# Kernel optimization log

Hardware: AMD Instinct MI355X
Metric: run time of the kernel (lower is better)

## Reference

```python
import jax, jax.numpy as jnp
import numpy as np

B, N, K = 4, 4096, 16
D_IN, D_T = 64, 128


def _linear_params(key, d_in, d_out, scale=0.02):
    kw, kb = jax.random.split(key)
    w = jax.random.normal(kw, (d_in, d_out), dtype=jnp.float32) * scale
    b = jax.random.normal(kb, (d_out,), dtype=jnp.float32) * scale
    return w, b


def setup_inputs() -> dict:
    key = jax.random.key(0)
    ks = jax.random.split(key, 12)
    x = jax.random.normal(ks[0], (B, N, D_IN), dtype=jnp.float32)
    pos = jax.random.normal(ks[1], (B, N, 3), dtype=jnp.float32)
    fc1_w, fc1_b = _linear_params(ks[2], D_IN, D_T)
    fc2_w, fc2_b = _linear_params(ks[3], D_T, D_IN)
    d1_w, d1_b = _linear_params(ks[4], 3, D_T)
    d2_w, d2_b = _linear_params(ks[5], D_T, D_T)
    g1_w, g1_b = _linear_params(ks[6], D_T, D_T)
    g2_w, g2_b = _linear_params(ks[7], D_T, D_T)
    wq = jax.random.normal(ks[8], (D_T, D_T), dtype=jnp.float32) * 0.02
    wk = jax.random.normal(ks[9], (D_T, D_T), dtype=jnp.float32) * 0.02
    wv = jax.random.normal(ks[10], (D_T, D_T), dtype=jnp.float32) * 0.02
    return dict(x=x, pos=pos, fc1_w=fc1_w, fc1_b=fc1_b, fc2_w=fc2_w, fc2_b=fc2_b,
                d1_w=d1_w, d1_b=d1_b, d2_w=d2_w, d2_b=d2_b,
                g1_w=g1_w, g1_b=g1_b, g2_w=g2_w, g2_b=g2_b,
                wq=wq, wk=wk, wv=wv)


def reference(x, pos, fc1_w, fc1_b, fc2_w, fc2_b, d1_w, d1_b, d2_w, d2_b,
              g1_w, g1_b, g2_w, g2_b, wq, wk, wv):
    # square_distance(pos, pos): [B, N, N]
    sq = jnp.sum(pos * pos, axis=-1)
    dists = sq[:, :, None] + sq[:, None, :] - 2.0 * jnp.einsum('bnc,bmc->bnm', pos, pos)
    knn_idx = jnp.argsort(dists, axis=-1)[:, :, :K]  # [B, N, K] int
    bidx = jnp.arange(B)[:, None, None]

    knn_pos = pos[bidx, knn_idx]                     # [B, N, K, 3]
    h = x @ fc1_w + fc1_b                            # [B, N, D_T]
    q = h @ wq                                       # [B, N, D_T]
    k = (h @ wk)[bidx, knn_idx]                      # [B, N, K, D_T]
    v = (h @ wv)[bidx, knn_idx]                      # [B, N, K, D_T]

    rel = pos[:, :, None, :] - knn_pos               # [B, N, K, 3]
    pos_enc = jax.nn.relu(rel @ d1_w + d1_b) @ d2_w + d2_b  # fc_delta

    a_in = q[:, :, None, :] - k + pos_enc
    attn = jax.nn.relu(a_in @ g1_w + g1_b) @ g2_w + g2_b    # fc_gamma
    attn = jax.nn.softmax(attn / np.sqrt(D_T).astype(np.float32), axis=-2)

    res = jnp.einsum('bmnf,bmnf->bmf', attn, v + pos_enc)   # [B, N, D_T]
    out = res @ fc2_w + fc2_b + x                           # [B, N, D_IN]
    return out, attn
```

## Files before the change

### kernel.cpp

```cpp
#include <hip/hip_runtime.h>
#include <float.h>

#define NPTS 4096
#define BN   16384
#define DT   128
#define DIN  64

typedef short v8s __attribute__((ext_vector_type(8)));
typedef float v4f __attribute__((ext_vector_type(4)));

__device__ __forceinline__ unsigned short f2bf(float f) {
    union { float f; unsigned u; } v; v.f = f;
    unsigned r = v.u + 0x7fff + ((v.u >> 16) & 1);
    return (unsigned short)(r >> 16);
}
__device__ __forceinline__ float bf2f(unsigned short s) {
    union { unsigned u; float f; } v; v.u = ((unsigned)s) << 16;
    return v.f;
}
__device__ __forceinline__ unsigned pack2(float lo, float hi) {
    unsigned r;
    asm("v_cvt_pk_bf16_f32 %0, %1, %2" : "=v"(r) : "v"(lo), "v"(hi));
    return r;
}

__global__ __launch_bounds__(256) void prep_kernel(
    const float* __restrict__ pos, const float* __restrict__ d2w,
    const float* __restrict__ g1w, const float* __restrict__ g2w,
    float4* __restrict__ pos4, unsigned short* __restrict__ wB) {
    int i = blockIdx.x * 256 + threadIdx.x;
    if (i < BN) {
        float p0 = pos[i*3], p1 = pos[i*3+1], p2 = pos[i*3+2];
        pos4[i] = make_float4(p0, p1, p2, fmaf(p2, p2, fmaf(p1, p1, p0*p0)));
    } else if (i < BN + 3*16384) {
        int e = i - BN; int m = e >> 14; e &= 16383;
        int k = e >> 7, n = e & 127;
        const float* W = (m == 0) ? d2w : (m == 1) ? g1w : g2w;
        float val = W[k*128 + n];
        int tile = n >> 4, nl = n & 15, ks = k >> 5, q = (k >> 3) & 3, j = k & 7;
        wB[m*16384 + ((tile*4 + ks)*64 + q*16 + nl)*8 + j] = f2bf(val);
    }
}

#define CSW(da,ia,db,ib) { bool sw_ = (da>db)||((da==db)&&(ia>ib)); \
    float td_=sw_?db:da, tD_=sw_?da:db; int ti_=sw_?ib:ia, tI_=sw_?ia:ib; \
    da=td_; db=tD_; ia=ti_; ib=tI_; }

__global__ __launch_bounds__(256, 4) void knn_kernel(const float4* __restrict__ pos4,
                                                     int* __restrict__ knnb) {
    __shared__ float scd[8][256];
    __shared__ int   sci[8][256];
    int t = threadIdx.x, lane = t & 63, w = t >> 6;
    int n0 = blockIdx.x * 8 + w * 2;
    int base = n0 & ~(NPTS - 1);
    float4 pa = pos4[n0], pb = pos4[n0 + 1];

    float mina = FLT_MAX, minb = FLT_MAX;
    for (int m = lane; m < NPTS; m += 64) {
        float4 c = pos4[base + m];
        float da = (pa.w + c.w) - 2.0f * fmaf(pa.z, c.z, fmaf(pa.y, c.y, pa.x*c.x));
        float db = (pb.w + c.w) - 2.0f * fmaf(pb.z, c.z, fmaf(pb.y, c.y, pb.x*c.x));
        mina = fminf(mina, da); minb = fminf(minb, db);
    }
    float taua, taub;
    {
        float va = mina, vb_ = minb;
#pragma unroll
        for (int k = 2; k <= 64; k <<= 1) {
#pragma unroll
            for (int j = k >> 1; j > 0; j >>= 1) {
                float oa = __shfl_xor(va, j, 64);
                float ob = __shfl_xor(vb_, j, 64);
                bool low = (lane & j) == 0;
                bool asc = (lane & k) == 0;
                va  = (low == asc) ? fminf(va, oa)  : fmaxf(va, oa);
                vb_ = (low == asc) ? fminf(vb_, ob) : fmaxf(vb_, ob);
            }
        }
        taua = __shfl(va, 15, 64);
        taub = __shfl(vb_, 15, 64);
    }
    int ca = 0, cb = 0;
    for (int m = lane; m < NPTS; m += 64) {
        float4 c = pos4[base + m];
        float da = (pa.w + c.w) - 2.0f * fmaf(pa.z, c.z, fmaf(pa.y, c.y, pa.x*c.x));
        float db = (pb.w + c.w) - 2.0f * fmaf(pb.z, c.z, fmaf(pb.y, c.y, pb.x*c.x));
        bool ta = da <= taua, tb_ = db <= taub;
        unsigned long long ma = __ballot(ta), mb = __ballot(tb_);
        unsigned long long lower = (1ull << lane) - 1ull;
        if (ta) {
            int p_ = ca + __popcll(ma & lower);
            if (p_ < 256) { scd[w*2][p_] = da; sci[w*2][p_] = base + m; }
        }
        if (tb_) {
            int p_ = cb + __popcll(mb & lower);
            if (p_ < 256) { scd[w*2+1][p_] = db; sci[w*2+1][p_] = base + m; }
        }
        ca += __popcll(ma); cb += __popcll(mb);
    }
    if (ca > 256) ca = 256;
    if (cb > 256) cb = 256;
    for (int i = ca + lane; i < 256; i += 64) { scd[w*2][i]   = FLT_MAX; sci[w*2][i]   = 0x7fffffff; }
    for (int i = cb + lane; i < 256; i += 64) { scd[w*2+1][i] = FLT_MAX; sci[w*2+1][i] = 0x7fffffff; }
    __syncthreads();

    for (int pt = 0; pt < 2; pt++) {
        int s = w*2 + pt;
        float4 dv = *(const float4*)&scd[s][lane*4];
        int4   iv = *(const int4*)&sci[s][lane*4];
        CSW(dv.x, iv.x, dv.y, iv.y);
        CSW(dv.z, iv.z, dv.w, iv.w);
        CSW(dv.x, iv.x, dv.z, iv.z);
        CSW(dv.y, iv.y, dv.w, iv.w);
        CSW(dv.y, iv.y, dv.z, iv.z);
        int p = 0, myres = 0;
        for (int r = 0; r < 16; r++) {
            float hd = p==0 ? dv.x : p==1 ? dv.y : p==2 ? dv.z : p==3 ? dv.w : FLT_MAX;
            int   hi = p==0 ? iv.x : p==1 ? iv.y : p==2 ? iv.z : p==3 ? iv.w : 0x7fffffff;
            float bd = hd; int bi = hi;
            for (int off = 32; off; off >>= 1) {
                float od = __shfl_xor(bd, off, 64);
                int   oi = __shfl_xor(bi, off, 64);
                if (od < bd || (od == bd && oi < bi)) { bd = od; bi = oi; }
            }
            if (hi == bi) p++;
            if (lane == r) myres = bi;
        }
        if (lane < 16) knnb[(n0 + pt)*16 + lane] = myres;
    }
}

__global__ __launch_bounds__(256) void feat_kernel(
    const float* __restrict__ x,
    const float* __restrict__ fc1w, const float* __restrict__ fc1b,
    const float* __restrict__ wq, const float* __restrict__ wk,
    const float* __restrict__ wv,
    unsigned short* __restrict__ qb, unsigned short* __restrict__ kb,
    unsigned short* __restrict__ vb) {
    __shared__ float xs[16][64];
    __shared__ float hs[16][128];
    int rb = blockIdx.x * 16;
    int t  = threadIdx.x;

    for (int i = t; i < 16*64; i += 256) xs[i>>6][i&63] = x[rb*64 + i];
    __syncthreads();

    int f4 = (t & 31) * 4;
    int r0 = (t >> 5) * 2, r1 = r0 + 1;
    float a0[4], a1[4];
#pragma unroll
    for (int jf = 0; jf < 4; jf++) { a0[jf] = fc1b[f4+jf]; a1[jf] = fc1b[f4+jf]; }
#pragma unroll 4
    for (int c = 0; c < 64; c += 4) {
        float s0[4], s1[4];
        *(float4*)s0 = *(const float4*)&xs[r0][c];
        *(float4*)s1 = *(const float4*)&xs[r1][c];
#pragma unroll
        for (int jc = 0; jc < 4; jc++) {
            float w[4];
            *(float4*)w = *(const float4*)&fc1w[(c+jc)*128 + f4];
#pragma unroll
            for (int jf = 0; jf < 4; jf++) {
                a0[jf] = fmaf(s0[jc], w[jf], a0[jf]);
                a1[jf] = fmaf(s1[jc], w[jf], a1[jf]);
            }
        }
    }
    *(float4*)&hs[r0][f4] = *(float4*)a0;
    *(float4*)&hs[r1][f4] = *(float4*)a1;
    __syncthreads();

    const float* Ws[3] = { wq, wk, wv };
    unsigned short* Os[3] = { qb, kb, vb };
    for (int mtx = 0; mtx < 3; mtx++) {
        const float* __restrict__ W = Ws[mtx];
#pragma unroll
        for (int jf = 0; jf < 4; jf++) { a0[jf] = 0.f; a1[jf] = 0.f; }
#pragma unroll 4
        for (int c = 0; c < 128; c += 4) {
            float s0[4], s1[4];
            *(float4*)s0 = *(const float4*)&hs[r0][c];
            *(float4*)s1 = *(const float4*)&hs[r1][c];
#pragma unroll
            for (int jc = 0; jc < 4; jc++) {
                float w[4];
                *(float4*)w = *(const float4*)&W[(c+jc)*128 + f4];
#pragma unroll
                for (int jf = 0; jf < 4; jf++) {
                    a0[jf] = fmaf(s0[jc], w[jf], a0[jf]);
                    a1[jf] = fmaf(s1[jc], w[jf], a1[jf]);
                }
            }
        }
        unsigned short* O = Os[mtx];
        uint2 s0v, s1v;
        s0v.x = pack2(a0[0], a0[1]); s0v.y = pack2(a0[2], a0[3]);
        s1v.x = pack2(a1[0], a1[1]); s1v.y = pack2(a1[2], a1[3]);
        *(uint2*)&O[(size_t)(rb+r0)*128 + f4] = s0v;
        *(uint2*)&O[(size_t)(rb+r1)*128 + f4] = s1v;
    }
}

__global__ __launch_bounds__(1024, 4) void fused_kernel(
    const float4* __restrict__ pos4, const int* __restrict__ knnb,
    const unsigned short* __restrict__ qb, const unsigned short* __restrict__ kb,
    const unsigned short* __restrict__ vb,
    const unsigned short* __restrict__ wB,
    const float* __restrict__ d1w, const float* __restrict__ d1b,
    const float* __restrict__ d2b, const float* __restrict__ g1b,
    const float* __restrict__ g2b,
    float* __restrict__ res, float* __restrict__ attn) {
    __shared__ unsigned short ws_[49152];
    __shared__ unsigned short tb[16][2048];
    int t = threadIdx.x;
    int lane = t & 63, w = t >> 6;
    int col = lane & 15, quad = lane >> 4;
    const float inv_s = 0.08838834764831845f;

    unsigned short* tw = &tb[w][0];
    float* twf = (float*)tw;

    {
        const uint4* src = (const uint4*)wB;
        uint4* dst = (uint4*)ws_;
        for (int i = t; i < 6144; i += 1024) dst[i] = src[i];
    }
    __syncthreads();

#pragma unroll
    for (int it = 0; it < 2; it++) {
        int n = (blockIdx.x * 16 + w) * 2 + it;
        {
            int jid = knnb[n*16 + col];

#pragma unroll
            for (int g = 0; g < 4; g++) {
                int kk2 = quad*4 + g;
                int jr2 = __shfl(jid, kk2);
                v8s kr = *(const v8s*)&kb[(size_t)jr2*128 + col*8];
                *(v8s*)&tw[kk2*128 + ((col ^ (kk2 & 7)) << 3)] = kr;
            }

            float4 pn = pos4[n];
            float4 pj = pos4[jid];
            float dx = pn.x - pj.x, dy = pn.y - pj.y, dz = pn.z - pj.z;

            v8s af[4];
#pragma unroll
            for (int ks = 0; ks < 4; ks++) {
                int fb = ks*32 + quad*8;
                float w0[8], w1[8], w2[8], bb[8];
                *(float4*)&w0[0] = *(const float4*)&d1w[fb];
                *(float4*)&w0[4] = *(const float4*)&d1w[fb+4];
                *(float4*)&w1[0] = *(const float4*)&d1w[128+fb];
                *(float4*)&w1[4] = *(const float4*)&d1w[128+fb+4];
                *(float4*)&w2[0] = *(const float4*)&d1w[256+fb];
                *(float4*)&w2[4] = *(const float4*)&d1w[256+fb+4];
                *(float4*)&bb[0] = *(const float4*)&d1b[fb];
                *(float4*)&bb[4] = *(const float4*)&d1b[fb+4];
                union { v8s s; unsigned u[4]; } afu;
#pragma unroll
                for (int j2 = 0; j2 < 4; j2++) {
                    float h0 = fmaf(dz, w2[j2*2],   fmaf(dy, w1[j2*2],   fmaf(dx, w0[j2*2],   bb[j2*2])));
                    float h1 = fmaf(dz, w2[j2*2+1], fmaf(dy, w1[j2*2+1], fmaf(dx, w0[j2*2+1], bb[j2*2+1])));
                    afu.u[j2] = pack2(fmaxf(h0, 0.0f), fmaxf(h1, 0.0f));
                }
                af[ks] = afu.s;
            }

            v8s frag[4];
            unsigned peP[16];

            {
                unsigned wo = 0; asm volatile("" : "+v"(wo));
#pragma unroll
                for (int tt = 0; tt < 8; tt++) {
                    v4f acc = {0.f, 0.f, 0.f, 0.f};
#pragma unroll
                    for (int ks = 0; ks < 4; ks++) {
                        v8s b = *(const v8s*)&ws_[wo + ((tt*4 + ks) << 9) + (lane << 3)];
                        acc = __builtin_amdgcn_mfma_f32_16x16x32_bf16(af[ks], b, acc, 0, 0, 0);
                    }
                    int cg = tt*16 + col;
                    float bias = d2b[cg];
                    float qv = bf2f(qb[(size_t)n*128 + cg]);
                    float pe0 = 0.f, pe1 = 0.f;
#pragma unroll
                    for (int r = 0; r < 4; r++) {
                        int kk = quad*4 + r;
                        int pidx = kk*128 + ((((cg >> 3) ^ (kk & 7))) << 3) + (cg & 6);
                        unsigned kp = *(const unsigned*)&tw[pidx];
                        float kv = bf2f((unsigned short)((lane & 1) ? (kp >> 16) : (kp & 0xffff)));
                        float pe = acc[r] + bias;
                        if (r == 0) pe0 = pe;
                        if (r == 1) { peP[tt*2]   = pack2(pe0, pe); }
                        if (r == 2) pe1 = pe;
                        if (r == 3) { peP[tt*2+1] = pack2(pe1, pe); }
                        float a  = qv - kv + pe;
                        float o = __shfl_xor(a, 1);
                        if ((lane & 1) == 0) *(unsigned*)&tw[pidx] = pack2(a, o);
                    }
                }
#pragma unroll
                for (int ks = 0; ks < 4; ks++)
                    frag[ks] = *(const v8s*)&tw[col*128 + ((((ks*4 + quad) ^ (col & 7))) << 3)];
            }

            {
                unsigned wo = 16384; asm volatile("" : "+v"(wo));
#pragma unroll
                for (int tt = 0; tt < 8; tt++) {
                    v4f acc = {0.f, 0.f, 0.f, 0.f};
#pragma unroll
                    for (int ks = 0; ks < 4; ks++) {
                        v8s b = *(const v8s*)&ws_[wo + ((tt*4 + ks) << 9) + (lane << 3)];
                        acc = __builtin_amdgcn_mfma_f32_16x16x32_bf16(frag[ks], b, acc, 0, 0, 0);
                    }
                    float bias = g1b[tt*16 + col];
#pragma unroll
                    for (int r = 0; r < 4; r++) {
                        float h = fmaxf(acc[r] + bias, 0.0f);
                        float o = __shfl_xor(h, 1);
                        if ((lane & 1) == 0) {
                            int kk = quad*4 + r;
                            int cg = tt*16 + col;
                            int idx = kk*128 + ((((cg >> 3) ^ (kk & 7))) << 3) + (cg & 7);
                            *(unsigned*)&tw[idx] = pack2(h, o);
                        }
                    }
                }
#pragma unroll
                for (int ks = 0; ks < 4; ks++)
                    frag[ks] = *(const v8s*)&tw[col*128 + ((((ks*4 + quad) ^ (col & 7))) << 3)];
            }

            {
#pragma unroll
                for (int g = 0; g < 4; g++) {
                    int kk2 = quad*4 + g;
                    int jr2 = __shfl(jid, kk2);
                    v8s vr = *(const v8s*)&vb[(size_t)jr2*128 + col*8];
                    *(v8s*)&tw[kk2*128 + ((col ^ (kk2 & 7)) << 3)] = vr;
                }

                unsigned wo = 32768; asm volatile("" : "+v"(wo));
                float av[8][4];
#pragma unroll
                for (int tt = 0; tt < 8; tt++) {
                    v4f acc = {0.f, 0.f, 0.f, 0.f};
#pragma unroll
                    for (int ks = 0; ks < 4; ks++) {
                        v8s b = *(const v8s*)&ws_[wo + ((tt*4 + ks) << 9) + (lane << 3)];
                        acc = __builtin_amdgcn_mfma_f32_16x16x32_bf16(frag[ks], b, acc, 0, 0, 0);
                    }
                    int cg = tt*16 + col;
                    float bias = g2b[cg];
                    float l[4];
                    float mx = -FLT_MAX;
#pragma unroll
                    for (int r = 0; r < 4; r++) {
                        l[r] = (acc[r] + bias) * inv_s;
                        mx = fmaxf(mx, l[r]);
                    }
                    mx = fmaxf(mx, __shfl_xor(mx, 16));
                    mx = fmaxf(mx, __shfl_xor(mx, 32));
                    float s = 0.f;
#pragma unroll
                    for (int r = 0; r < 4; r++) { l[r] = __expf(l[r] - mx); s += l[r]; }
                    s += __shfl_xor(s, 16);
                    s += __shfl_xor(s, 32);
                    float rs = 1.0f / s;
                    float rp = 0.f;
#pragma unroll
                    for (int r = 0; r < 4; r++) {
                        int kk = quad*4 + r;
                        int pidx = kk*128 + ((((cg >> 3) ^ (kk & 7))) << 3) + (cg & 6);
                        unsigned vp = *(const unsigned*)&tw[pidx];
                        float vv = bf2f((unsigned short)((lane & 1) ? (vp >> 16) : (vp & 0xffff)));
                        unsigned pp = peP[tt*2 + (r >> 1)];
                        float pe = bf2f((unsigned short)((r & 1) ? (pp >> 16) : (pp & 0xffff)));
                        float a_ = l[r] * rs;
                        av[tt][r] = a_;
                        rp = fmaf(a_, vv + pe, rp);
                    }
                    rp += __shfl_xor(rp, 16);
                    rp += __shfl_xor(rp, 32);
                    if (lane < 16) res[(size_t)n*128 + cg] = rp;
                }

#pragma unroll
                for (int h = 0; h < 2; h++) {
#pragma unroll
                    for (int tt2 = 0; tt2 < 4; tt2++) {
#pragma unroll
                        for (int r = 0; r < 4; r++) {
                            int kk = quad*4 + r;
                            twf[kk*64 + ((tt2*16 + col) ^ ((kk & 4) << 2))] = av[h*4 + tt2][r];
                        }
                    }
#pragma unroll
                    for (int s4 = 0; s4 < 4; s4++) {
                        int kk = s4*4 + quad;
                        int c4 = col*4;
                        float4 a4 = *(const float4*)&twf[kk*64 + (c4 ^ ((kk & 4) << 2))];
                        *(float4*)&attn[(size_t)(n*16 + kk)*128 + h*64 + c4] = a4;
                    }
                }
            }
        }
    }
}

__global__ __launch_bounds__(256) void epi_kernel(
    const float* __restrict__ res, const float* __restrict__ fc2w,
    const float* __restrict__ fc2b, const float* __restrict__ x,
    float* __restrict__ out) {
    __shared__ float fw[128][64];
    __shared__ float rs[16][128];
    int t = threadIdx.x;
    int rb = blockIdx.x * 16;
    for (int i = t; i < 8192; i += 256) fw[i >> 6][i & 63] = fc2w[i];
    for (int i = t; i < 2048; i += 256) rs[i >> 7][i & 127] = res[(size_t)rb*128 + i];
    __syncthreads();

    int o = t & 63, g = t >> 6;
#pragma unroll
    for (int rr = 0; rr < 4; rr++) {
        int lr = rr*4 + g;
        int n = rb + lr;
        float a0 = 0.f, a1 = 0.f, a2 = 0.f, a3 = 0.f;
#pragma unroll 8
        for (int c = 0; c < 128; c += 4) {
            a0 = fmaf(rs[lr][c],   fw[c][o],   a0);
            a1 = fmaf(rs[lr][c+1], fw[c+1][o], a1);
            a2 = fmaf(rs[lr][c+2], fw[c+2][o], a2);
            a3 = fmaf(rs[lr][c+3], fw[c+3][o], a3);
        }
        out[(size_t)n*64 + o] = (a0 + a1) + (a2 + a3) + fc2b[o] + x[(size_t)n*64 + o];
    }
}

extern "C" void kernel_launch(void* const* d_in, const int* in_sizes, int n_in,
                              void* d_out, int out_size, void* d_ws, size_t ws_size,
                              hipStream_t stream) {
    (void)in_sizes; (void)n_in; (void)out_size; (void)ws_size;
    const float* x    = (const float*)d_in[0];
    const float* pos  = (const float*)d_in[1];
    const float* fc1w = (const float*)d_in[2];
    const float* fc1b = (const float*)d_in[3];
    const float* fc2w = (const float*)d_in[4];
    const float* fc2b = (const float*)d_in[5];
    const float* d1w  = (const float*)d_in[6];
    const float* d1b  = (const float*)d_in[7];
    const float* d2w  = (const float*)d_in[8];
    const float* d2b  = (const float*)d_in[9];
    const float* g1w  = (const float*)d_in[10];
    const float* g1b  = (const float*)d_in[11];
    const float* g2w  = (const float*)d_in[12];
    const float* g2b  = (const float*)d_in[13];
    const float* wq   = (const float*)d_in[14];
    const float* wk   = (const float*)d_in[15];
    const float* wv   = (const float*)d_in[16];

    float* out      = (float*)d_out;
    float* attn_out = out + (size_t)BN * DIN;

    char* W = (char*)d_ws;
    float4*         pos4  = (float4*)(W + 0);
    unsigned short* wB    = (unsigned short*)(W + 262144);
    int*            knnb  = (int*)(W + 376832);
    unsigned short* qb    = (unsigned short*)(W + 1441792);
    unsigned short* kb    = (unsigned short*)(W + 5636096);
    unsigned short* vb    = (unsigned short*)(W + 9830400);
    float*          res   = (float*)(W + 14024704);

    prep_kernel<<<256, 256, 0, stream>>>(pos, d2w, g1w, g2w, pos4, wB);
    knn_kernel<<<2048, 256, 0, stream>>>(pos4, knnb);
    feat_kernel<<<1024, 256, 0, stream>>>(x, fc1w, fc1b, wq, wk, wv, qb, kb, vb);
    fused_kernel<<<512, 1024, 0, stream>>>(pos4, knnb, qb, kb, vb, wB, d1w, d1b,
                                           d2b, g1b, g2b, res, attn_out);
    epi_kernel<<<1024, 256, 0, stream>>>(res, fc2w, fc2b, x, out);
}
```

Measured before the change: 409.8 us.

## Merge prep, kNN and feature kernels into one block-dispatched front kernel

Folds the three independent front-end kernels (pos/weight prep, kNN selection, QKV projection) into a single launch whose block index selects the role, so they can overlap and launch overhead drops. The kNN path now reads raw pos (stride 3) and recomputes squared norms instead of depending on pos4 produced by the prep stage. The main fused kernel's occupancy hint changes from launch_bounds min-blocks to an explicit waves-per-EU attribute. The cost is less coalesced pos loads and extra arithmetic in the kNN loops, plus a larger shared-memory footprint for the feature blocks.

```diff
diff --git a/kernel.cpp b/kernel.cpp
--- a/kernel.cpp
+++ b/kernel.cpp
@@ -24,167 +24,135 @@
     return r;
 }
 
-__global__ __launch_bounds__(256) void prep_kernel(
-    const float* __restrict__ pos, const float* __restrict__ d2w,
-    const float* __restrict__ g1w, const float* __restrict__ g2w,
-    float4* __restrict__ pos4, unsigned short* __restrict__ wB) {
-    int i = blockIdx.x * 256 + threadIdx.x;
-    if (i < BN) {
-        float p0 = pos[i*3], p1 = pos[i*3+1], p2 = pos[i*3+2];
-        pos4[i] = make_float4(p0, p1, p2, fmaf(p2, p2, fmaf(p1, p1, p0*p0)));
-    } else if (i < BN + 3*16384) {
-        int e = i - BN; int m = e >> 14; e &= 16383;
-        int k = e >> 7, n = e & 127;
-        const float* W = (m == 0) ? d2w : (m == 1) ? g1w : g2w;
-        float val = W[k*128 + n];
-        int tile = n >> 4, nl = n & 15, ks = k >> 5, q = (k >> 3) & 3, j = k & 7;
-        wB[m*16384 + ((tile*4 + ks)*64 + q*16 + nl)*8 + j] = f2bf(val);
-    }
-}
-
 #define CSW(da,ia,db,ib) { bool sw_ = (da>db)||((da==db)&&(ia>ib)); \
     float td_=sw_?db:da, tD_=sw_?da:db; int ti_=sw_?ib:ia, tI_=sw_?ia:ib; \
     da=td_; db=tD_; ia=ti_; ib=tI_; }
 
-__global__ __launch_bounds__(256, 4) void knn_kernel(const float4* __restrict__ pos4,
-                                                     int* __restrict__ knnb) {
-    __shared__ float scd[8][256];
-    __shared__ int   sci[8][256];
-    int t = threadIdx.x, lane = t & 63, w = t >> 6;
-    int n0 = blockIdx.x * 8 + w * 2;
-    int base = n0 & ~(NPTS - 1);
-    float4 pa = pos4[n0], pb = pos4[n0 + 1];
-
-    float mina = FLT_MAX, minb = FLT_MAX;
-    for (int m = lane; m < NPTS; m += 64) {
-        float4 c = pos4[base + m];
-        float da = (pa.w + c.w) - 2.0f * fmaf(pa.z, c.z, fmaf(pa.y, c.y, pa.x*c.x));
-        float db = (pb.w + c.w) - 2.0f * fmaf(pb.z, c.z, fmaf(pb.y, c.y, pb.x*c.x));
-        mina = fminf(mina, da); minb = fminf(minb, db);
-    }
-    float taua, taub;
-    {
-        float va = mina, vb_ = minb;
-#pragma unroll
-        for (int k = 2; k <= 64; k <<= 1) {
-#pragma unroll
-            for (int j = k >> 1; j > 0; j >>= 1) {
-                float oa = __shfl_xor(va, j, 64);
-                float ob = __shfl_xor(vb_, j, 64);
-                bool low = (lane & j) == 0;
-                bool asc = (lane & k) == 0;
-                va  = (low == asc) ? fminf(va, oa)  : fmaxf(va, oa);
-                vb_ = (low == asc) ? fminf(vb_, ob) : fmaxf(vb_, ob);
-            }
-        }
-        taua = __shfl(va, 15, 64);
-        taub = __shfl(vb_, 15, 64);
-    }
-    int ca = 0, cb = 0;
-    for (int m = lane; m < NPTS; m += 64) {
-        float4 c = pos4[base + m];
-        float da = (pa.w + c.w) - 2.0f * fmaf(pa.z, c.z, fmaf(pa.y, c.y, pa.x*c.x));
-        float db = (pb.w + c.w) - 2.0f * fmaf(pb.z, c.z, fmaf(pb.y, c.y, pb.x*c.x));
-        bool ta = da <= taua, tb_ = db <= taub;
-        unsigned long long ma = __ballot(ta), mb = __ballot(tb_);
-        unsigned long long lower = (1ull << lane) - 1ull;
-        if (ta) {
-            int p_ = ca + __popcll(ma & lower);
-            if (p_ < 256) { scd[w*2][p_] = da; sci[w*2][p_] = base + m; }
-        }
-        if (tb_) {
-            int p_ = cb + __popcll(mb & lower);
-            if (p_ < 256) { scd[w*2+1][p_] = db; sci[w*2+1][p_] = base + m; }
-        }
-        ca += __popcll(ma); cb += __popcll(mb);
-    }
-    if (ca > 256) ca = 256;
-    if (cb > 256) cb = 256;
-    for (int i = ca + lane; i < 256; i += 64) { scd[w*2][i]   = FLT_MAX; sci[w*2][i]   = 0x7fffffff; }
-    for (int i = cb + lane; i < 256; i += 64) { scd[w*2+1][i] = FLT_MAX; sci[w*2+1][i] = 0x7fffffff; }
-    __syncthreads();
-
-    for (int pt = 0; pt < 2; pt++) {
-        int s = w*2 + pt;
-        float4 dv = *(const float4*)&scd[s][lane*4];
-        int4   iv = *(const int4*)&sci[s][lane*4];
-        CSW(dv.x, iv.x, dv.y, iv.y);
-        CSW(dv.z, iv.z, dv.w, iv.w);
-        CSW(dv.x, iv.x, dv.z, iv.z);
-        CSW(dv.y, iv.y, dv.w, iv.w);
-        CSW(dv.y, iv.y, dv.z, iv.z);
-        int p = 0, myres = 0;
-        for (int r = 0; r < 16; r++) {
-            float hd = p==0 ? dv.x : p==1 ? dv.y : p==2 ? dv.z : p==3 ? dv.w : FLT_MAX;
-            int   hi = p==0 ? iv.x : p==1 ? iv.y : p==2 ? iv.z : p==3 ? iv.w : 0x7fffffff;
-            float bd = hd; int bi = hi;
-            for (int off = 32; off; off >>= 1) {
-                float od = __shfl_xor(bd, off, 64);
-                int   oi = __shfl_xor(bi, off, 64);
-                if (od < bd || (od == bd && oi < bi)) { bd = od; bi = oi; }
-            }
-            if (hi == bi) p++;
-            if (lane == r) myres = bi;
-        }
-        if (lane < 16) knnb[(n0 + pt)*16 + lane] = myres;
-    }
-}
-
-__global__ __launch_bounds__(256) void feat_kernel(
-    const float* __restrict__ x,
+__global__ __launch_bounds__(256) void front_kernel(
+    const float* __restrict__ pos, const float* __restrict__ x,
     const float* __restrict__ fc1w, const float* __restrict__ fc1b,
     const float* __restrict__ wq, const float* __restrict__ wk,
     const float* __restrict__ wv,
+    const float* __restrict__ d2w, const float* __restrict__ g1w,
+    const float* __restrict__ g2w,
+    float4* __restrict__ pos4, unsigned short* __restrict__ wB,
+    int* __restrict__ knnb,
     unsigned short* __restrict__ qb, unsigned short* __restrict__ kb,
     unsigned short* __restrict__ vb) {
-    __shared__ float xs[16][64];
-    __shared__ float hs[16][128];
-    int rb = blockIdx.x * 16;
-    int t  = threadIdx.x;
-
-    for (int i = t; i < 16*64; i += 256) xs[i>>6][i&63] = x[rb*64 + i];
-    __syncthreads();
-
-    int f4 = (t & 31) * 4;
-    int r0 = (t >> 5) * 2, r1 = r0 + 1;
-    float a0[4], a1[4];
-#pragma unroll
-    for (int jf = 0; jf < 4; jf++) { a0[jf] = fc1b[f4+jf]; a1[jf] = fc1b[f4+jf]; }
+    __shared__ float smem[4096];
+    int bid = blockIdx.x;
+    int t = threadIdx.x;
+
+    if (bid < 2048) {
+        float (*scd)[256] = (float(*)[256])smem;
+        int   (*sci)[256] = (int(*)[256])(smem + 2048);
+        int lane = t & 63, w = t >> 6;
+        int n0 = bid * 8 + w * 2;
+        int base = n0 & ~(NPTS - 1);
+        float pax = pos[n0*3], pay = pos[n0*3+1], paz = pos[n0*3+2];
+        float paw = fmaf(paz, paz, fmaf(pay, pay, pax*pax));
+        float pbx = pos[n0*3+3], pby = pos[n0*3+4], pbz = pos[n0*3+5];
+        float pbw = fmaf(pbz, pbz, fmaf(pby, pby, pbx*pbx));
+
+        float mina = FLT_MAX, minb = FLT_MAX;
+        for (int m = lane; m < NPTS; m += 64) {
+            const float* cp = &pos[(size_t)(base + m)*3];
+            float cx = cp[0], cy = cp[1], cz = cp[2];
+            float cw = fmaf(cz, cz, fmaf(cy, cy, cx*cx));
+            float da = (paw + cw) - 2.0f * fmaf(paz, cz, fmaf(pay, cy, pax*cx));
+            float db = (pbw + cw) - 2.0f * fmaf(pbz, cz, fmaf(pby, cy, pbx*cx));
+            mina = fminf(mina, da); minb = fminf(minb, db);
+        }
+        float taua, taub;
+        {
+            float va = mina, vb_ = minb;
+#pragma unroll
+            for (int k = 2; k <= 64; k <<= 1) {
+#pragma unroll
+                for (int j = k >> 1; j > 0; j >>= 1) {
+                    float oa = __shfl_xor(va, j, 64);
+                    float ob = __shfl_xor(vb_, j, 64);
+                    bool low = (lane & j) == 0;
+                    bool asc = (lane & k) == 0;
+                    va  = (low == asc) ? fminf(va, oa)  : fmaxf(va, oa);
+                    vb_ = (low == asc) ? fminf(vb_, ob) : fmaxf(vb_, ob);
+                }
+            }
+            taua = __shfl(va, 15, 64);
+            taub = __shfl(vb_, 15, 64);
+        }
+        int ca = 0, cb = 0;
+        for (int m = lane; m < NPTS; m += 64) {
+            const float* cp = &pos[(size_t)(base + m)*3];
+            float cx = cp[0], cy = cp[1], cz = cp[2];
+            float cw = fmaf(cz, cz, fmaf(cy, cy, cx*cx));
+            float da = (paw + cw) - 2.0f * fmaf(paz, cz, fmaf(pay, cy, pax*cx));
+            float db = (pbw + cw) - 2.0f * fmaf(pbz, cz, fmaf(pby, cy, pbx*cx));
+            bool ta = da <= taua, tb_ = db <= taub;
+            unsigned long long ma = __ballot(ta), mb = __ballot(tb_);
+            unsigned long long lower = (1ull << lane) - 1ull;
+            if (ta) {
+                int p_ = ca + __popcll(ma & lower);
+                if (p_ < 256) { scd[w*2][p_] = da; sci[w*2][p_] = base + m; }
+            }
+            if (tb_) {
+                int p_ = cb + __popcll(mb & lower);
+                if (p_ < 256) { scd[w*2+1][p_] = db; sci[w*2+1][p_] = base + m; }
+            }
+            ca += __popcll(ma); cb += __popcll(mb);
+        }
+        if (ca > 256) ca = 256;
+        if (cb > 256) cb = 256;
+        for (int i = ca + lane; i < 256; i += 64) { scd[w*2][i]   = FLT_MAX; sci[w*2][i]   = 0x7fffffff; }
+        for (int i = cb + lane; i < 256; i += 64) { scd[w*2+1][i] = FLT_MAX; sci[w*2+1][i] = 0x7fffffff; }
+        __syncthreads();
+
+        for (int pt = 0; pt < 2; pt++) {
+            int s = w*2 + pt;
+            float4 dv = *(const float4*)&scd[s][lane*4];
+            int4   iv = *(const int4*)&sci[s][lane*4];
+            CSW(dv.x, iv.x, dv.y, iv.y);
+            CSW(dv.z, iv.z, dv.w, iv.w);
+            CSW(dv.x, iv.x, dv.z, iv.z);
+            CSW(dv.y, iv.y, dv.w, iv.w);
+            CSW(dv.y, iv.y, dv.z, iv.z);
+            int p = 0, myres = 0;
+            for (int r = 0; r < 16; r++) {
+                float hd = p==0 ? dv.x : p==1 ? dv.y : p==2 ? dv.z : p==3 ? dv.w : FLT_MAX;
+                int   hi = p==0 ? iv.x : p==1 ? iv.y : p==2 ? iv.z : p==3 ? iv.w : 0x7fffffff;
+                float bd = hd; int bi = hi;
+                for (int off = 32; off; off >>= 1) {
+                    float od = __shfl_xor(bd, off, 64);
+                    int   oi = __shfl_xor(bi, off, 64);
+                    if (od < bd || (od == bd && oi < bi)) { bd = od; bi = oi; }
+                }
+                if (hi == bi) p++;
+                if (lane == r) myres = bi;
+            }
+            if (lane < 16) knnb[(n0 + pt)*16 + lane] = myres;
+        }
+    } else if (bid < 3072) {
+        float (*xs)[64]  = (float(*)[64])smem;
+        float (*hs)[128] = (float(*)[128])(smem + 1024);
+        int rb = (bid - 2048) * 16;
+
+        for (int i = t; i < 16*64; i += 256) xs[i>>6][i&63] = x[rb*64 + i];
+        __syncthreads();
+
+        int f4 = (t & 31) * 4;
+        int r0 = (t >> 5) * 2, r1 = r0 + 1;
+        float a0[4], a1[4];
+#pragma unroll
+        for (int jf = 0; jf < 4; jf++) { a0[jf] = fc1b[f4+jf]; a1[jf] = fc1b[f4+jf]; }
 #pragma unroll 4
-    for (int c = 0; c < 64; c += 4) {
-        float s0[4], s1[4];
-        *(float4*)s0 = *(const float4*)&xs[r0][c];
-        *(float4*)s1 = *(const float4*)&xs[r1][c];
-#pragma unroll
-        for (int jc = 0; jc < 4; jc++) {
-            float w[4];
-            *(float4*)w = *(const float4*)&fc1w[(c+jc)*128 + f4];
-#pragma unroll
-            for (int jf = 0; jf < 4; jf++) {
-                a0[jf] = fmaf(s0[jc], w[jf], a0[jf]);
-                a1[jf] = fmaf(s1[jc], w[jf], a1[jf]);
-            }
-        }
-    }
-    *(float4*)&hs[r0][f4] = *(float4*)a0;
-    *(float4*)&hs[r1][f4] = *(float4*)a1;
-    __syncthreads();
-
-    const float* Ws[3] = { wq, wk, wv };
-    unsigned short* Os[3] = { qb, kb, vb };
-    for (int mtx = 0; mtx < 3; mtx++) {
-        const float* __restrict__ W = Ws[mtx];
-#pragma unroll
-        for (int jf = 0; jf < 4; jf++) { a0[jf] = 0.f; a1[jf] = 0.f; }
-#pragma unroll 4
-        for (int c = 0; c < 128; c += 4) {
+        for (int c = 0; c < 64; c += 4) {
             float s0[4], s1[4];
-            *(float4*)s0 = *(const float4*)&hs[r0][c];
-            *(float4*)s1 = *(const float4*)&hs[r1][c];
+            *(float4*)s0 = *(const float4*)&xs[r0][c];
+            *(float4*)s1 = *(const float4*)&xs[r1][c];
 #pragma unroll
             for (int jc = 0; jc < 4; jc++) {
                 float w[4];
-                *(float4*)w = *(const float4*)&W[(c+jc)*128 + f4];
+                *(float4*)w = *(const float4*)&fc1w[(c+jc)*128 + f4];
 #pragma unroll
                 for (int jf = 0; jf < 4; jf++) {
                     a0[jf] = fmaf(s0[jc], w[jf], a0[jf]);
@@ -192,16 +160,57 @@
                 }
             }
         }
-        unsigned short* O = Os[mtx];
-        uint2 s0v, s1v;
-        s0v.x = pack2(a0[0], a0[1]); s0v.y = pack2(a0[2], a0[3]);
-        s1v.x = pack2(a1[0], a1[1]); s1v.y = pack2(a1[2], a1[3]);
-        *(uint2*)&O[(size_t)(rb+r0)*128 + f4] = s0v;
-        *(uint2*)&O[(size_t)(rb+r1)*128 + f4] = s1v;
+        *(float4*)&hs[r0][f4] = *(float4*)a0;
+        *(float4*)&hs[r1][f4] = *(float4*)a1;
+        __syncthreads();
+
+        const float* Ws[3] = { wq, wk, wv };
+        unsigned short* Os[3] = { qb, kb, vb };
+        for (int mtx = 0; mtx < 3; mtx++) {
+            const float* __restrict__ W = Ws[mtx];
+#pragma unroll
+            for (int jf = 0; jf < 4; jf++) { a0[jf] = 0.f; a1[jf] = 0.f; }
+#pragma unroll 4
+            for (int c = 0; c < 128; c += 4) {
+                float s0[4], s1[4];
+                *(float4*)s0 = *(const float4*)&hs[r0][c];
+                *(float4*)s1 = *(const float4*)&hs[r1][c];
+#pragma unroll
+                for (int jc = 0; jc < 4; jc++) {
+                    float w[4];
+                    *(float4*)w = *(const float4*)&W[(c+jc)*128 + f4];
+#pragma unroll
+                    for (int jf = 0; jf < 4; jf++) {
+                        a0[jf] = fmaf(s0[jc], w[jf], a0[jf]);
+                        a1[jf] = fmaf(s1[jc], w[jf], a1[jf]);
+                    }
+                }
+            }
+            unsigned short* O = Os[mtx];
+            uint2 s0v, s1v;
+            s0v.x = pack2(a0[0], a0[1]); s0v.y = pack2(a0[2], a0[3]);
+            s1v.x = pack2(a1[0], a1[1]); s1v.y = pack2(a1[2], a1[3]);
+            *(uint2*)&O[(size_t)(rb+r0)*128 + f4] = s0v;
+            *(uint2*)&O[(size_t)(rb+r1)*128 + f4] = s1v;
+        }
+    } else {
+        int i = (bid - 3072) * 256 + t;
+        if (i < BN) {
+            float p0 = pos[i*3], p1 = pos[i*3+1], p2 = pos[i*3+2];
+            pos4[i] = make_float4(p0, p1, p2, fmaf(p2, p2, fmaf(p1, p1, p0*p0)));
+        } else {
+            int e = i - BN; int m = e >> 14; e &= 16383;
+            int k = e >> 7, n = e & 127;
+            const float* W = (m == 0) ? d2w : (m == 1) ? g1w : g2w;
+            float val = W[k*128 + n];
+            int tile = n >> 4, nl = n & 15, ks = k >> 5, q = (k >> 3) & 3, j = k & 7;
+            wB[m*16384 + ((tile*4 + ks)*64 + q*16 + nl)*8 + j] = f2bf(val);
+        }
     }
 }
 
-__global__ __launch_bounds__(1024, 4) void fused_kernel(
+__global__ __attribute__((amdgpu_waves_per_eu(4, 4)))
+__launch_bounds__(1024) void fused_kernel(
     const float4* __restrict__ pos4, const int* __restrict__ knnb,
     const unsigned short* __restrict__ qb, const unsigned short* __restrict__ kb,
     const unsigned short* __restrict__ vb,
@@ -474,9 +483,9 @@
     unsigned short* vb    = (unsigned short*)(W + 9830400);
     float*          res   = (float*)(W + 14024704);
 
-    prep_kernel<<<256, 256, 0, stream>>>(pos, d2w, g1w, g2w, pos4, wB);
-    knn_kernel<<<2048, 256, 0, stream>>>(pos4, knnb);
-    feat_kernel<<<1024, 256, 0, stream>>>(x, fc1w, fc1b, wq, wk, wv, qb, kb, vb);
+    front_kernel<<<3328, 256, 0, stream>>>(pos, x, fc1w, fc1b, wq, wk, wv,
+                                           d2w, g1w, g2w,
+                                           pos4, wB, knnb, qb, kb, vb);
     fused_kernel<<<512, 1024, 0, stream>>>(pos4, knnb, qb, kb, vb, wB, d1w, d1b,
                                            d2b, g1b, g2b, res, attn_out);
     epi_kernel<<<1024, 256, 0, stream>>>(res, fc2w, fc2b, x, out);
```

Result: slower. 435.8 us (+6.4%).
